# Kernel optimization log

Measured on AMD Instinct MI355X. Metric: run time of the kernel, lower is better.

## Reference

```python
import jax, jax.numpy as jnp
import numpy as np

B, N, H = 4, 2048, 128
NUM_HEADS = 4
HEAD_DIM = H // NUM_HEADS
SCALE = np.sqrt(HEAD_DIM).astype(np.float32)


def setup_inputs() -> dict:
    key = jax.random.key(0)
    ks = jax.random.split(key, 16)

    def lin_w(k, o, i):
        return jax.random.normal(k, (o, i), dtype=jnp.float32) / np.sqrt(i).astype(np.float32)

    def lin_b(k, o, i):
        return jax.random.uniform(k, (o,), dtype=jnp.float32, minval=-1, maxval=1) / np.sqrt(i).astype(np.float32)

    return {
        "h": jax.random.normal(ks[0], (B, N, H), dtype=jnp.float32),
        "coords": jax.random.normal(ks[1], (B, N, 3), dtype=jnp.float32),
        "mask": jnp.ones((B, N), dtype=bool),
        "Wq": lin_w(ks[2], H, H), "bq": lin_b(ks[3], H, H),
        "Wk": lin_w(ks[4], H, H), "bk": lin_b(ks[5], H, H),
        "Wv": lin_w(ks[6], H, H), "bv": lin_b(ks[7], H, H),
        "Wo": lin_w(ks[8], H, H), "bo": lin_b(ks[9], H, H),
        "Wc1": lin_w(ks[10], H, H), "bc1": lin_b(ks[11], H, H),
        "Wc2": lin_w(ks[12], 1, H),  # no bias
    }


def reference(h, coords, mask, Wq, bq, Wk, bk, Wv, bv, Wo, bo, Wc1, bc1, Wc2):
    b, n, hd = h.shape
    # projections (torch Linear: y = x @ W.T + b), split heads
    Q = (h @ Wq.T + bq).reshape(b, n, NUM_HEADS, HEAD_DIM)
    K = (h @ Wk.T + bk).reshape(b, n, NUM_HEADS, HEAD_DIM)
    V = (h @ Wv.T + bv).reshape(b, n, NUM_HEADS, HEAD_DIM)

    # scores: (B, heads, N, N)
    scores = jnp.einsum('bnhd,bmhd->bhnm', Q, K) / SCALE
    # mask over keys (last dim), as in torch: mask (B,1,1,N)
    scores = jnp.where(mask[:, None, None, :], scores, -jnp.inf)
    attn = jax.nn.softmax(scores, axis=-1)  # dropout is identity in eval

    h_attn = jnp.einsum('bhnm,bmhd->bnhd', attn, V).reshape(b, n, hd)
    h_out = h_attn @ Wo.T + bo

    # scalar gate per node, softmax over nodes (dim=1)
    cw = jax.nn.silu(h @ Wc1.T + bc1) @ Wc2.T  # (B, N, 1)
    cw = jax.nn.softmax(cw, axis=1)

    # coords_update[b,n] = sum_m a[n,m]*(coords[n]-coords[m])
    #                    = (sum_m a[n,m]) * coords[n] - A @ coords
    # (avoids materializing the B x N x N x 3 coords_diff tensor; same math)
    attn_mean = attn.mean(axis=1)  # (B, N, N)
    row_sum = attn_mean.sum(axis=-1, keepdims=True)  # (B, N, 1)
    coords_update = row_sum * coords - jnp.einsum('bnm,bmd->bnd', attn_mean, coords)
    coords_out = coords + coords_update * cw
    return h_out, coords_out
```

## Files before the change

kernel.cpp:

```cpp
#include <hip/hip_runtime.h>
#include <hip/hip_bf16.h>


typedef __bf16    bf16x8 __attribute__((ext_vector_type(8)));
typedef __bf16    bf16x4 __attribute__((ext_vector_type(4)));
typedef _Float16  f16x8  __attribute__((ext_vector_type(8)));
typedef _Float16  f16x4  __attribute__((ext_vector_type(4)));
typedef float     f32x4  __attribute__((ext_vector_type(4)));

constexpr float QK_E2 = 0.2550316861118708f;

__device__ inline float fast_exp2(float x) {
#if __has_builtin(__builtin_amdgcn_exp2f)
    return __builtin_amdgcn_exp2f(x);
#else
    return exp2f(x);
#endif
}

__device__ inline bf16x8 cvt8(const float* p) {
    float4 a = *(const float4*)p;
    float4 b = *(const float4*)(p + 4);
    bf16x8 o;
    o[0] = (__bf16)a.x; o[1] = (__bf16)a.y; o[2] = (__bf16)a.z; o[3] = (__bf16)a.w;
    o[4] = (__bf16)b.x; o[5] = (__bf16)b.y; o[6] = (__bf16)b.z; o[7] = (__bf16)b.w;
    return o;
}

__global__ __launch_bounds__(256) void prep(
    const float* __restrict__ coords,
    const float* __restrict__ Wq, const float* __restrict__ Wk,
    const float* __restrict__ Wv, const float* __restrict__ Wc1,
    const float* __restrict__ Wo,
    __hip_bfloat16* __restrict__ Wsw, _Float16* __restrict__ Csw)
{
    const int tid = threadIdx.x, blk = blockIdx.x;
    if (blk < 40) {
        int lin = blk * 256 + tid;
        int lane = lin & 63, rest = lin >> 6;
        int sub = rest & 7, mk = rest >> 3;
        int mat = mk >> 2, k4 = mk & 3;
        int col = lane & 15, quad = lane >> 4;
        const float* W = (mat == 0) ? Wq : (mat == 1) ? Wk :
                         (mat == 2) ? Wv : (mat == 3) ? Wc1 : Wo;
        bf16x8 o = cvt8(W + (size_t)(sub * 16 + col) * 128 + k4 * 32 + quad * 8);
        *(bf16x8*)(Wsw + (size_t)lin * 8) = o;
    } else {
        int lin = (blk - 40) * 256 + tid;
        int lane = lin & 63, bk2 = lin >> 6;
        int col = lane & 15, quad = lane >> 4;
        f16x4 o;
        if (col < 3) {
            #pragma unroll
            for (int j = 0; j < 4; ++j)
                o[j] = (_Float16)coords[((size_t)bk2 * 16 + quad * 4 + j) * 3 + col];
        } else if (col == 3) {
            o[0] = o[1] = o[2] = o[3] = (_Float16)1.f;
        } else {
            o[0] = o[1] = o[2] = o[3] = (_Float16)0.f;
        }
        *(f16x4*)(Csw + (size_t)lin * 4) = o;
    }
}

__global__ __launch_bounds__(256) void proj_mfma(
    const float* __restrict__ h, const __hip_bfloat16* __restrict__ Wsw,
    const float* __restrict__ bq, const float* __restrict__ bk,
    const float* __restrict__ bv, const float* __restrict__ bc1,
    const float* __restrict__ Wc2,
    __hip_bfloat16* __restrict__ Qb, __hip_bfloat16* __restrict__ Kb,
    _Float16* __restrict__ Vsw, float* __restrict__ g)
{
    __shared__ float sh[16 * 132];

    const int tid = threadIdx.x;
    const int wave = tid >> 6, lane = tid & 63;
    const int col = lane & 15, quad = lane >> 4;
    const int row0 = blockIdx.x * 16;
    const int b = row0 >> 11, n0 = row0 & 2047;

    {
        int idx = tid * 8, r = idx >> 7, c0 = idx & 127;
        float4 v0 = *(const float4*)(h + (size_t)(row0 + r) * 128 + c0);
        float4 v1 = *(const float4*)(h + (size_t)(row0 + r) * 128 + c0 + 4);
        *(float4*)(sh + r * 132 + c0) = v0;
        *(float4*)(sh + r * 132 + c0 + 4) = v1;
    }
    __syncthreads();

    bf16x8 a[4];
    #pragma unroll
    for (int k4 = 0; k4 < 4; ++k4)
        a[k4] = cvt8(sh + col * 132 + k4 * 32 + quad * 8);

    f32x4 acc[8];
    #pragma unroll
    for (int s = 0; s < 8; ++s) acc[s] = (f32x4){0.f, 0.f, 0.f, 0.f};

    #pragma unroll
    for (int k4 = 0; k4 < 4; ++k4) {
        #pragma unroll
        for (int sub = 0; sub < 8; ++sub) {
            bf16x8 bf = *(const bf16x8*)(Wsw +
                (((size_t)(wave * 4 + k4) * 8 + sub) * 64 + lane) * 8);
            acc[sub] = __builtin_amdgcn_mfma_f32_16x16x32_bf16(a[k4], bf, acc[sub], 0, 0, 0);
        }
    }

    if (wave == 0) {
        #pragma unroll
        for (int sub = 0; sub < 8; ++sub) {
            int c = sub * 16 + col, head = c >> 5, d = c & 31;
            float bias = bq[c];
            size_t base = (size_t)(b * 4 + head) * 2048 + n0 + quad * 4;
            #pragma unroll
            for (int r = 0; r < 4; ++r)
                Qb[(base + r) * 32 + d] = __float2bfloat16((acc[sub][r] + bias) * QK_E2);
        }
    } else if (wave == 1) {
        #pragma unroll
        for (int sub = 0; sub < 8; ++sub) {
            int c = sub * 16 + col, head = c >> 5, d = c & 31;
            float bias = bk[c];
            size_t base = (size_t)(b * 4 + head) * 2048 + n0 + quad * 4;
            #pragma unroll
            for (int r = 0; r < 4; ++r)
                Kb[(base + r) * 32 + d] = __float2bfloat16(acc[sub][r] + bias);
        }
    } else if (wave == 2) {
        const int kc = n0 >> 4;
        #pragma unroll
        for (int sub = 0; sub < 8; ++sub) {
            int c = sub * 16 + col, head = c >> 5;
            float bias = bv[c];
            f16x4 vv;
            #pragma unroll
            for (int r = 0; r < 4; ++r) vv[r] = (_Float16)(acc[sub][r] + bias);
            *(f16x4*)(Vsw + (((size_t)(b * 4 + head) * 128 + kc) * 64
                             + quad * 16 + col) * 8 + (sub & 1) * 4) = vv;
        }
    } else {
        float gsum[4] = {0.f, 0.f, 0.f, 0.f};
        #pragma unroll
        for (int sub = 0; sub < 8; ++sub) {
            int c = sub * 16 + col;
            float bias = bc1[c], w2 = Wc2[c];
            #pragma unroll
            for (int r = 0; r < 4; ++r) {
                float x = acc[sub][r] + bias;
                gsum[r] += (x / (1.f + __expf(-x))) * w2;
            }
        }
        #pragma unroll
        for (int r = 0; r < 4; ++r) {
            gsum[r] += __shfl_xor(gsum[r], 1);
            gsum[r] += __shfl_xor(gsum[r], 2);
            gsum[r] += __shfl_xor(gsum[r], 4);
            gsum[r] += __shfl_xor(gsum[r], 8);
            if (col == 0) g[row0 + quad * 4 + r] = gsum[r];
        }
    }
}

__global__ __launch_bounds__(512, 2) void attn_out(
    const __hip_bfloat16* __restrict__ Qb, const __hip_bfloat16* __restrict__ Kb,
    const _Float16* __restrict__ Vsw, const _Float16* __restrict__ Csw,
    const __hip_bfloat16* __restrict__ Wsw, const float* __restrict__ g,
    const float* __restrict__ coords, const float* __restrict__ bo,
    float* __restrict__ out_h, float* __restrict__ out_c)
{
    __shared__ f32x4 red[6][8][64];
    __shared__ __bf16 hsw_s[2][4][64][8];
    __shared__ float ach_s[2][16][4][3];
    __shared__ float gsred[16];

    const int tid = threadIdx.x;
    const int wave = tid >> 6, lane = tid & 63;
    const int col = lane & 15, quad = lane >> 4;

    const int bid = blockIdx.x;
    const int xcd = bid & 7, slot = bid >> 3;
    const int b = xcd >> 1;
    const int q0 = ((xcd & 1) * 32 + slot) * 32;
    const int head = wave >> 1, half = wave & 1;
    const int bh = b * 4 + head;

    const float* gb = g + (size_t)b * 2048;
    float4 gv = *(const float4*)(gb + tid * 4);
    float mx = fmaxf(fmaxf(gv.x, gv.y), fmaxf(gv.z, gv.w));
    #pragma unroll
    for (int off = 32; off; off >>= 1) mx = fmaxf(mx, __shfl_xor(mx, off));
    if (lane == 0) gsred[wave] = mx;
    __syncthreads();
    float M = gsred[0];
    #pragma unroll
    for (int w = 1; w < 8; ++w) M = fmaxf(M, gsred[w]);
    float sum = __expf(gv.x - M) + __expf(gv.y - M)
              + __expf(gv.z - M) + __expf(gv.w - M);
    #pragma unroll
    for (int off = 32; off; off >>= 1) sum += __shfl_xor(sum, off);
    if (lane == 0) gsred[8 + wave] = sum;
    __syncthreads();
    float ssum = gsred[8];
    #pragma unroll
    for (int w = 9; w < 16; ++w) ssum += gsred[w];
    const float invS = 1.f / ssum;

    const __hip_bfloat16* Qp = Qb + ((size_t)bh * 2048 + q0) * 32;
    const bf16x8 qA = *(const bf16x8*)(Qp + (size_t)col * 32 + quad * 8);
    const bf16x8 qB = *(const bf16x8*)(Qp + (size_t)(16 + col) * 32 + quad * 8);

    const __hip_bfloat16* Kp = Kb + ((size_t)bh * 2048 + half * 1024) * 32;
    const _Float16* Vp = Vsw + ((size_t)bh * 128 + half * 64) * 512;
    const _Float16* Cp = Csw + ((size_t)b * 128 + half * 64) * 256;

    f32x4 oLoA = {0,0,0,0}, oHiA = {0,0,0,0}, cA = {0,0,0,0};
    f32x4 oLoB = {0,0,0,0}, oHiB = {0,0,0,0}, cB = {0,0,0,0};
    const f32x4 fz = {0,0,0,0};

    bf16x8 kbuf[4]; f16x8 vbuf[4]; f16x4 cbuf[4];
    #pragma unroll
    for (int s = 0; s < 3; ++s) {
        kbuf[s] = *(const bf16x8*)(Kp + (size_t)(s * 16 + col) * 32 + quad * 8);
        vbuf[s] = *(const f16x8*)(Vp + (size_t)s * 512 + lane * 8);
        cbuf[s] = *(const f16x4*)(Cp + (size_t)s * 256 + lane * 4);
    }

    #pragma unroll 4
    for (int it = 0; it < 64; ++it) {
        const int pf = (it + 3 < 64) ? (it + 3) : 63;
        const int ws2 = (it + 3) & 3;
        kbuf[ws2] = *(const bf16x8*)(Kp + (size_t)(pf * 16 + col) * 32 + quad * 8);
        vbuf[ws2] = *(const f16x8*)(Vp + (size_t)pf * 512 + lane * 8);
        cbuf[ws2] = *(const f16x4*)(Cp + (size_t)pf * 256 + lane * 4);

        const int rs = it & 3;
        bf16x8 kf = kbuf[rs];
        f16x8 v8  = vbuf[rs];
        f16x4 cf  = cbuf[rs];

        f32x4 sA = __builtin_amdgcn_mfma_f32_16x16x32_bf16(kf, qA, fz, 0, 0, 0);
        f32x4 sB = __builtin_amdgcn_mfma_f32_16x16x32_bf16(kf, qB, fz, 0, 0, 0);

        f16x4 pA, pB;
        #pragma unroll
        for (int r = 0; r < 4; ++r) {
            pA[r] = (_Float16)fast_exp2(sA[r]);
            pB[r] = (_Float16)fast_exp2(sB[r]);
        }

        f16x4 vlo = {v8[0], v8[1], v8[2], v8[3]};
        f16x4 vhi = {v8[4], v8[5], v8[6], v8[7]};

        oLoA = __builtin_amdgcn_mfma_f32_16x16x16f16(vlo, pA, oLoA, 0, 0, 0);
        oHiA = __builtin_amdgcn_mfma_f32_16x16x16f16(vhi, pA, oHiA, 0, 0, 0);
        cA   = __builtin_amdgcn_mfma_f32_16x16x16f16(cf,  pA, cA,   0, 0, 0);
        oLoB = __builtin_amdgcn_mfma_f32_16x16x16f16(vlo, pB, oLoB, 0, 0, 0);
        oHiB = __builtin_amdgcn_mfma_f32_16x16x16f16(vhi, pB, oHiB, 0, 0, 0);
        cB   = __builtin_amdgcn_mfma_f32_16x16x16f16(cf,  pB, cB,   0, 0, 0);
    }

    red[0][wave][lane] = oLoA; red[1][wave][lane] = oHiA; red[2][wave][lane] = cA;
    red[3][wave][lane] = oLoB; red[4][wave][lane] = oHiB; red[5][wave][lane] = cB;
    __syncthreads();

    {
        const int h = wave >> 1, gq = wave & 1;
        const int base = gq * 3;
        const int w0 = h * 2, w1 = h * 2 + 1;
        f32x4 oLo = red[base+0][w0][lane] + red[base+0][w1][lane];
        f32x4 oHi = red[base+1][w0][lane] + red[base+1][w1][lane];
        f32x4 cc  = red[base+2][w0][lane] + red[base+2][w1][lane];
        float l = red[base+2][w0][col][3] + red[base+2][w1][col][3];
        float invl = 1.f / l;

        bf16x4 lo4, hi4;
        #pragma unroll
        for (int r = 0; r < 4; ++r) {
            lo4[r] = (__bf16)(oLo[r] * invl);
            hi4[r] = (__bf16)(oHi[r] * invl);
        }
        *(bf16x4*)(&hsw_s[gq][h][(quad >> 1) * 16 + col][(quad & 1) * 4]) = lo4;
        *(bf16x4*)(&hsw_s[gq][h][(2 + (quad >> 1)) * 16 + col][(quad & 1) * 4]) = hi4;

        if (quad == 0) {
            #pragma unroll
            for (int r = 0; r < 3; ++r)
                ach_s[gq][col][h][r] = cc[r] * invl;
        }
    }
    __syncthreads();

    {
        const int tl = wave >> 2, cg = wave & 3;
        bf16x8 a[4];
        #pragma unroll
        for (int k4 = 0; k4 < 4; ++k4)
            a[k4] = *(const bf16x8*)(&hsw_s[tl][k4][lane][0]);

        f32x4 acc[2] = {{0.f,0.f,0.f,0.f}, {0.f,0.f,0.f,0.f}};
        #pragma unroll
        for (int k4 = 0; k4 < 4; ++k4) {
            #pragma unroll
            for (int sub = 0; sub < 2; ++sub) {
                int c16 = cg * 2 + sub;
                bf16x8 bf = *(const bf16x8*)(Wsw +
                    (((size_t)(16 + k4) * 8 + c16) * 64 + lane) * 8);
                acc[sub] = __builtin_amdgcn_mfma_f32_16x16x32_bf16(a[k4], bf, acc[sub], 0, 0, 0);
            }
        }

        const size_t row_base = (size_t)b * 2048 + q0 + tl * 16;
        #pragma unroll
        for (int sub = 0; sub < 2; ++sub) {
            int c = (cg * 2 + sub) * 16 + col;
            float bias = bo[c];
            #pragma unroll
            for (int r = 0; r < 4; ++r)
                out_h[(row_base + quad * 4 + r) * 128 + c] = acc[sub][r] + bias;
        }
    }

    if (tid < 96) {
        int r = tid / 3, d2 = tid % 3;
        int nloc = q0 + r;
        float am = 0.25f * (ach_s[r >> 4][r & 15][0][d2] + ach_s[r >> 4][r & 15][1][d2]
                          + ach_s[r >> 4][r & 15][2][d2] + ach_s[r >> 4][r & 15][3][d2]);
        float cwv = __expf(gb[nloc] - M) * invS;
        size_t row = (size_t)b * 2048 + nloc;
        float c = coords[row * 3 + d2];
        out_c[row * 3 + d2] = c + (c - am) * cwv;
    }
}

extern "C" void kernel_launch(void* const* d_in, const int* in_sizes, int n_in,
                              void* d_out, int out_size, void* d_ws, size_t ws_size,
                              hipStream_t stream)
{
    (void)in_sizes; (void)n_in; (void)out_size; (void)ws_size;

    const float* h      = (const float*)d_in[0];
    const float* coords = (const float*)d_in[1];
    const float* Wq  = (const float*)d_in[3];  const float* bq  = (const float*)d_in[4];
    const float* Wk  = (const float*)d_in[5];  const float* bk  = (const float*)d_in[6];
    const float* Wv  = (const float*)d_in[7];  const float* bv  = (const float*)d_in[8];
    const float* Wo  = (const float*)d_in[9];  const float* bo  = (const float*)d_in[10];
    const float* Wc1 = (const float*)d_in[11]; const float* bc1 = (const float*)d_in[12];
    const float* Wc2 = (const float*)d_in[13];

    __hip_bfloat16* Qb   = (__hip_bfloat16*)d_ws;
    __hip_bfloat16* Kb   = Qb + 1048576;
    __hip_bfloat16* Wsw  = Kb + 1048576;
    _Float16* Vsw = (_Float16*)(Wsw + 81920);
    _Float16* Csw = Vsw + 1048576;
    float* g   = (float*)(Csw + 131072);

    float* out_h = (float*)d_out;
    float* out_c = out_h + (size_t)4 * 2048 * 128;

    hipLaunchKernelGGL(prep, dim3(168), dim3(256), 0, stream,
                       coords, Wq, Wk, Wv, Wc1, Wo, Wsw, Csw);
    hipLaunchKernelGGL(proj_mfma, dim3(512), dim3(256), 0, stream,
                       h, Wsw, bq, bk, bv, bc1, Wc2, Qb, Kb, Vsw, g);
    hipLaunchKernelGGL(attn_out, dim3(256), dim3(512), 0, stream,
                       Qb, Kb, Vsw, Csw, Wsw, g, coords, bo, out_h, out_c);
}
```

Baseline: 109.9 us.

## Fold coords packing into projection kernel, defer gate softmax, pack exp conversions

The coords-to-f16 packing moves out of the prep kernel into an otherwise idle wave of the projection kernel, so prep shrinks to the 40 weight-swizzle blocks. In the attention kernel, the gate-softmax max/sum reduction moves after the main loop, where it shares the existing barriers instead of adding two up front. The exp results are now packed to f16 pairs with cvt_pkrtz, which rounds toward zero instead of to nearest. Prefetch addressing is simplified to precomputed lane pointers and the clamp is dropped, so the last iterations read a little past each tile into neighbouring workspace data that is never used.

```diff
diff --git a/kernel.cpp b/kernel.cpp
--- a/kernel.cpp
+++ b/kernel.cpp
@@ -6,6 +6,7 @@
 typedef __bf16    bf16x4 __attribute__((ext_vector_type(4)));
 typedef _Float16  f16x8  __attribute__((ext_vector_type(8)));
 typedef _Float16  f16x4  __attribute__((ext_vector_type(4)));
+typedef _Float16  f16x2  __attribute__((ext_vector_type(2)));
 typedef float     f32x4  __attribute__((ext_vector_type(4)));
 
 constexpr float QK_E2 = 0.2550316861118708f;
@@ -16,6 +17,12 @@
 #else
     return exp2f(x);
 #endif
+}
+
+__device__ inline f16x4 pack4(float a, float b, float c, float d) {
+    f16x2 lo = __builtin_bit_cast(f16x2, __builtin_amdgcn_cvt_pkrtz(a, b));
+    f16x2 hi = __builtin_bit_cast(f16x2, __builtin_amdgcn_cvt_pkrtz(c, d));
+    return __builtin_shufflevector(lo, hi, 0, 1, 2, 3);
 }
 
 __device__ inline bf16x8 cvt8(const float* p) {
@@ -28,55 +35,39 @@
 }
 
 __global__ __launch_bounds__(256) void prep(
-    const float* __restrict__ coords,
     const float* __restrict__ Wq, const float* __restrict__ Wk,
     const float* __restrict__ Wv, const float* __restrict__ Wc1,
-    const float* __restrict__ Wo,
-    __hip_bfloat16* __restrict__ Wsw, _Float16* __restrict__ Csw)
+    const float* __restrict__ Wo, __hip_bfloat16* __restrict__ Wsw)
 {
     const int tid = threadIdx.x, blk = blockIdx.x;
-    if (blk < 40) {
-        int lin = blk * 256 + tid;
-        int lane = lin & 63, rest = lin >> 6;
-        int sub = rest & 7, mk = rest >> 3;
-        int mat = mk >> 2, k4 = mk & 3;
-        int col = lane & 15, quad = lane >> 4;
-        const float* W = (mat == 0) ? Wq : (mat == 1) ? Wk :
-                         (mat == 2) ? Wv : (mat == 3) ? Wc1 : Wo;
-        bf16x8 o = cvt8(W + (size_t)(sub * 16 + col) * 128 + k4 * 32 + quad * 8);
-        *(bf16x8*)(Wsw + (size_t)lin * 8) = o;
-    } else {
-        int lin = (blk - 40) * 256 + tid;
-        int lane = lin & 63, bk2 = lin >> 6;
-        int col = lane & 15, quad = lane >> 4;
-        f16x4 o;
-        if (col < 3) {
-            #pragma unroll
-            for (int j = 0; j < 4; ++j)
-                o[j] = (_Float16)coords[((size_t)bk2 * 16 + quad * 4 + j) * 3 + col];
-        } else if (col == 3) {
-            o[0] = o[1] = o[2] = o[3] = (_Float16)1.f;
-        } else {
-            o[0] = o[1] = o[2] = o[3] = (_Float16)0.f;
-        }
-        *(f16x4*)(Csw + (size_t)lin * 4) = o;
-    }
+    int lin = blk * 256 + tid;
+    int lane = lin & 63, rest = lin >> 6;
+    int sub = rest & 7, mk = rest >> 3;
+    int mat = mk >> 2, k4 = mk & 3;
+    int col = lane & 15, quad = lane >> 4;
+    const float* W = (mat == 0) ? Wq : (mat == 1) ? Wk :
+                     (mat == 2) ? Wv : (mat == 3) ? Wc1 : Wo;
+    bf16x8 o = cvt8(W + (size_t)(sub * 16 + col) * 128 + k4 * 32 + quad * 8);
+    *(bf16x8*)(Wsw + (size_t)lin * 8) = o;
 }
 
 __global__ __launch_bounds__(256) void proj_mfma(
-    const float* __restrict__ h, const __hip_bfloat16* __restrict__ Wsw,
+    const float* __restrict__ h, const float* __restrict__ coords,
+    const __hip_bfloat16* __restrict__ Wsw,
     const float* __restrict__ bq, const float* __restrict__ bk,
     const float* __restrict__ bv, const float* __restrict__ bc1,
     const float* __restrict__ Wc2,
     __hip_bfloat16* __restrict__ Qb, __hip_bfloat16* __restrict__ Kb,
-    _Float16* __restrict__ Vsw, float* __restrict__ g)
+    _Float16* __restrict__ Vsw, _Float16* __restrict__ Csw,
+    float* __restrict__ g)
 {
     __shared__ float sh[16 * 132];
 
     const int tid = threadIdx.x;
     const int wave = tid >> 6, lane = tid & 63;
     const int col = lane & 15, quad = lane >> 4;
-    const int row0 = blockIdx.x * 16;
+    const int blk = blockIdx.x;
+    const int row0 = blk * 16;
     const int b = row0 >> 11, n0 = row0 & 2047;
 
     {
@@ -85,6 +76,20 @@
         float4 v1 = *(const float4*)(h + (size_t)(row0 + r) * 128 + c0 + 4);
         *(float4*)(sh + r * 132 + c0) = v0;
         *(float4*)(sh + r * 132 + c0 + 4) = v1;
+    }
+
+    if (wave == 3) {
+        f16x4 o;
+        if (col < 3) {
+            #pragma unroll
+            for (int j = 0; j < 4; ++j)
+                o[j] = (_Float16)coords[(size_t)(row0 + quad * 4 + j) * 3 + col];
+        } else if (col == 3) {
+            o[0] = o[1] = o[2] = o[3] = (_Float16)1.f;
+        } else {
+            o[0] = o[1] = o[2] = o[3] = (_Float16)0.f;
+        }
+        *(f16x4*)(Csw + ((size_t)blk * 64 + lane) * 4) = o;
     }
     __syncthreads();
 
@@ -185,34 +190,14 @@
     const int head = wave >> 1, half = wave & 1;
     const int bh = b * 4 + head;
 
-    const float* gb = g + (size_t)b * 2048;
-    float4 gv = *(const float4*)(gb + tid * 4);
-    float mx = fmaxf(fmaxf(gv.x, gv.y), fmaxf(gv.z, gv.w));
-    #pragma unroll
-    for (int off = 32; off; off >>= 1) mx = fmaxf(mx, __shfl_xor(mx, off));
-    if (lane == 0) gsred[wave] = mx;
-    __syncthreads();
-    float M = gsred[0];
-    #pragma unroll
-    for (int w = 1; w < 8; ++w) M = fmaxf(M, gsred[w]);
-    float sum = __expf(gv.x - M) + __expf(gv.y - M)
-              + __expf(gv.z - M) + __expf(gv.w - M);
-    #pragma unroll
-    for (int off = 32; off; off >>= 1) sum += __shfl_xor(sum, off);
-    if (lane == 0) gsred[8 + wave] = sum;
-    __syncthreads();
-    float ssum = gsred[8];
-    #pragma unroll
-    for (int w = 9; w < 16; ++w) ssum += gsred[w];
-    const float invS = 1.f / ssum;
-
     const __hip_bfloat16* Qp = Qb + ((size_t)bh * 2048 + q0) * 32;
     const bf16x8 qA = *(const bf16x8*)(Qp + (size_t)col * 32 + quad * 8);
     const bf16x8 qB = *(const bf16x8*)(Qp + (size_t)(16 + col) * 32 + quad * 8);
 
-    const __hip_bfloat16* Kp = Kb + ((size_t)bh * 2048 + half * 1024) * 32;
-    const _Float16* Vp = Vsw + ((size_t)bh * 128 + half * 64) * 512;
-    const _Float16* Cp = Csw + ((size_t)b * 128 + half * 64) * 256;
+    const __hip_bfloat16* Kl = Kb + ((size_t)bh * 2048 + half * 1024 + col) * 32
+                               + quad * 8;
+    const _Float16* Vl = Vsw + ((size_t)bh * 128 + half * 64) * 512 + lane * 8;
+    const _Float16* Cl = Csw + ((size_t)b * 128 + half * 64) * 256 + lane * 4;
 
     f32x4 oLoA = {0,0,0,0}, oHiA = {0,0,0,0}, cA = {0,0,0,0};
     f32x4 oLoB = {0,0,0,0}, oHiB = {0,0,0,0}, cB = {0,0,0,0};
@@ -221,18 +206,17 @@
     bf16x8 kbuf[4]; f16x8 vbuf[4]; f16x4 cbuf[4];
     #pragma unroll
     for (int s = 0; s < 3; ++s) {
-        kbuf[s] = *(const bf16x8*)(Kp + (size_t)(s * 16 + col) * 32 + quad * 8);
-        vbuf[s] = *(const f16x8*)(Vp + (size_t)s * 512 + lane * 8);
-        cbuf[s] = *(const f16x4*)(Cp + (size_t)s * 256 + lane * 4);
+        kbuf[s] = *(const bf16x8*)(Kl + (size_t)s * 512);
+        vbuf[s] = *(const f16x8*)(Vl + (size_t)s * 512);
+        cbuf[s] = *(const f16x4*)(Cl + (size_t)s * 256);
     }
 
     #pragma unroll 4
     for (int it = 0; it < 64; ++it) {
-        const int pf = (it + 3 < 64) ? (it + 3) : 63;
-        const int ws2 = (it + 3) & 3;
-        kbuf[ws2] = *(const bf16x8*)(Kp + (size_t)(pf * 16 + col) * 32 + quad * 8);
-        vbuf[ws2] = *(const f16x8*)(Vp + (size_t)pf * 512 + lane * 8);
-        cbuf[ws2] = *(const f16x4*)(Cp + (size_t)pf * 256 + lane * 4);
+        const int pf = it + 3, ws2 = pf & 3;
+        kbuf[ws2] = *(const bf16x8*)(Kl + (size_t)pf * 512);
+        vbuf[ws2] = *(const f16x8*)(Vl + (size_t)pf * 512);
+        cbuf[ws2] = *(const f16x4*)(Cl + (size_t)pf * 256);
 
         const int rs = it & 3;
         bf16x8 kf = kbuf[rs];
@@ -242,12 +226,10 @@
         f32x4 sA = __builtin_amdgcn_mfma_f32_16x16x32_bf16(kf, qA, fz, 0, 0, 0);
         f32x4 sB = __builtin_amdgcn_mfma_f32_16x16x32_bf16(kf, qB, fz, 0, 0, 0);
 
-        f16x4 pA, pB;
-        #pragma unroll
-        for (int r = 0; r < 4; ++r) {
-            pA[r] = (_Float16)fast_exp2(sA[r]);
-            pB[r] = (_Float16)fast_exp2(sB[r]);
-        }
+        f16x4 pA = pack4(fast_exp2(sA[0]), fast_exp2(sA[1]),
+                         fast_exp2(sA[2]), fast_exp2(sA[3]));
+        f16x4 pB = pack4(fast_exp2(sB[0]), fast_exp2(sB[1]),
+                         fast_exp2(sB[2]), fast_exp2(sB[3]));
 
         f16x4 vlo = {v8[0], v8[1], v8[2], v8[3]};
         f16x4 vhi = {v8[4], v8[5], v8[6], v8[7]};
@@ -262,7 +244,24 @@
 
     red[0][wave][lane] = oLoA; red[1][wave][lane] = oHiA; red[2][wave][lane] = cA;
     red[3][wave][lane] = oLoB; red[4][wave][lane] = oHiB; red[5][wave][lane] = cB;
+
+    const float* gb = g + (size_t)b * 2048;
+    float4 gv = *(const float4*)(gb + tid * 4);
+    float mx = fmaxf(fmaxf(gv.x, gv.y), fmaxf(gv.z, gv.w));
+    #pragma unroll
+    for (int off = 32; off; off >>= 1) mx = fmaxf(mx, __shfl_xor(mx, off));
+    if (lane == 0) gsred[wave] = mx;
+
     __syncthreads();
+
+    float M = gsred[0];
+    #pragma unroll
+    for (int w = 1; w < 8; ++w) M = fmaxf(M, gsred[w]);
+    float sum = __expf(gv.x - M) + __expf(gv.y - M)
+              + __expf(gv.z - M) + __expf(gv.w - M);
+    #pragma unroll
+    for (int off = 32; off; off >>= 1) sum += __shfl_xor(sum, off);
+    if (lane == 0) gsred[8 + wave] = sum;
 
     {
         const int h = wave >> 1, gq = wave & 1;
@@ -291,6 +290,11 @@
     }
     __syncthreads();
 
+    float ssum = gsred[8];
+    #pragma unroll
+    for (int w = 9; w < 16; ++w) ssum += gsred[w];
+    const float invS = 1.f / ssum;
+
     {
         const int tl = wave >> 2, cg = wave & 3;
         bf16x8 a[4];
@@ -358,10 +362,10 @@
     float* out_h = (float*)d_out;
     float* out_c = out_h + (size_t)4 * 2048 * 128;
 
-    hipLaunchKernelGGL(prep, dim3(168), dim3(256), 0, stream,
-                       coords, Wq, Wk, Wv, Wc1, Wo, Wsw, Csw);
+    hipLaunchKernelGGL(prep, dim3(40), dim3(256), 0, stream,
+                       Wq, Wk, Wv, Wc1, Wo, Wsw);
     hipLaunchKernelGGL(proj_mfma, dim3(512), dim3(256), 0, stream,
-                       h, Wsw, bq, bk, bv, bc1, Wc2, Qb, Kb, Vsw, g);
+                       h, coords, Wsw, bq, bk, bv, bc1, Wc2, Qb, Kb, Vsw, Csw, g);
     hipLaunchKernelGGL(attn_out, dim3(256), dim3(512), 0, stream,
                        Qb, Kb, Vsw, Csw, Wsw, g, coords, bo, out_h, out_c);
 }
```

After: 109.2 us. About the same (-0.6%).
